# Optimization experiments

Hardware: AMD Instinct MI355X
Metric: run time of the kernel (lower is better)

The kernel has to match this reference:

```python
import jax, jax.numpy as jnp
import numpy as np

B, S, E, H = 2, 2048, 2048, 16
D = E // H  # head_out == qk_out (linformer_factor=1, attention_groups=0)
NEG = -1e30


def alibi_slopes(n_heads):
    # standard ALiBi slopes: 2^(-8*h/n_heads) for h = 1..n_heads
    return jnp.asarray(2.0 ** (-8.0 * np.arange(1, n_heads + 1) / n_heads), dtype=jnp.float32)


def setup_inputs() -> dict:
    key = jax.random.key(0)
    ks = jax.random.split(key, 5)
    sc = 0.02
    return {
        "x": jax.random.normal(ks[0], (B, S, E), dtype=jnp.float32),
        "Wq": jax.random.normal(ks[1], (E, E), dtype=jnp.float32) * sc,
        "Wk": jax.random.normal(ks[2], (E, E), dtype=jnp.float32) * sc,
        "Wv": jax.random.normal(ks[3], (E, E), dtype=jnp.float32) * sc,
        "Wo": jax.random.normal(ks[4], (E, E), dtype=jnp.float32) * sc,
        "bo": jnp.zeros((E,), dtype=jnp.float32),
    }


def reference(x, Wq, Wk, Wv, Wo, bo):
    b, s, e = x.shape
    # projections, split heads: [b, H, s, D]
    q = (x @ Wq).reshape(b, s, H, D).transpose(0, 2, 1, 3)
    k = (x @ Wk).reshape(b, s, H, D).transpose(0, 2, 1, 3)
    v = (x @ Wv).reshape(b, s, H, D).transpose(0, 2, 1, 3)
    scores = jnp.einsum("bhqd,bhkd->bhqk", q, k)
    # causal mask applied BEFORE scaling (as in original calc_attention)
    i = jnp.arange(s)[:, None]
    j = jnp.arange(s)[None, :]
    causal = j <= i  # [s, s]
    scores = jnp.where(causal[None, None], scores, NEG)
    # ALiBi bias: slope_h * (j - i), added before scaling
    bias = alibi_slopes(H)[:, None, None] * (j - i).astype(jnp.float32)  # [H, s, s]
    scores = scores + bias[None]
    scores = scores / jnp.sqrt(jnp.float32(D))
    w = jax.nn.softmax(scores, axis=-1)  # dropout rate 0.0 -> identity
    ctx = jnp.einsum("bhqk,bhkd->bqhd", w, v).reshape(b, s, e)
    return ctx @ Wo + bo
```

## Files before the change

### kernel.cpp

```cpp
#include <hip/hip_runtime.h>

#define BB 2
#define SS 2048
#define EE 2048
#define HH 16
#define DD 128
#define SE (3 * EE)

typedef __bf16 bf16x8 __attribute__((ext_vector_type(8)));
typedef unsigned short u16x8 __attribute__((ext_vector_type(8)));
typedef float f32x4 __attribute__((ext_vector_type(4)));

__device__ __forceinline__ unsigned short f32_to_bf16(float f) {
  unsigned int u = __builtin_bit_cast(unsigned int, f);
  u += 0x7FFFu + ((u >> 16) & 1u);
  return (unsigned short)(u >> 16);
}

__device__ __forceinline__ void gll16(const void* g, const void* lds) {
  __builtin_amdgcn_global_load_lds(
      (const __attribute__((address_space(1))) unsigned int*)g,
      (__attribute__((address_space(3))) unsigned int*)lds, 16, 0, 0);
}

__device__ __forceinline__ bf16x8 lds_frag(const unsigned short* p) {
  return __builtin_bit_cast(bf16x8, *(const u16x8*)p);
}

__global__ void k_cast_bf16(const float* __restrict__ x, unsigned short* __restrict__ y) {
  int i = blockIdx.x * 256 + threadIdx.x;
  float4 v = ((const float4*)x)[i];
  ushort4 o;
  o.x = f32_to_bf16(v.x); o.y = f32_to_bf16(v.y);
  o.z = f32_to_bf16(v.z); o.w = f32_to_bf16(v.w);
  ((ushort4*)y)[i] = o;
}

__global__ void k_transpose_w4(const float* __restrict__ W0, const float* __restrict__ W1,
                               const float* __restrict__ W2, const float* __restrict__ W3,
                               unsigned short* __restrict__ WtBase) {
  const float* W = blockIdx.z == 0 ? W0 : blockIdx.z == 1 ? W1 : blockIdx.z == 2 ? W2 : W3;
  unsigned short* Wt = WtBase + (size_t)blockIdx.z * EE * EE;
  __shared__ float tile[32][33];
  int n0 = blockIdx.x * 32, k0 = blockIdx.y * 32;
  int t = threadIdx.x, r = t >> 5, c = t & 31;
  for (int i = 0; i < 32; i += 8)
    tile[r + i][c] = W[(size_t)(k0 + r + i) * EE + n0 + c];
  __syncthreads();
  for (int i = 0; i < 32; i += 8)
    Wt[(size_t)(n0 + r + i) * EE + k0 + c] = f32_to_bf16(tile[c][r + i]);
}

__global__ void k_transpose_v(const unsigned short* __restrict__ QKV, unsigned short* __restrict__ Vt) {
  __shared__ unsigned short tile[32][33];
  int s0 = blockIdx.x * 32, d0 = blockIdx.y * 32, bh = blockIdx.z;
  int b = bh >> 4, h = bh & 15;
  int t = threadIdx.x, r = t >> 5, c = t & 31;
  for (int i = 0; i < 32; i += 8)
    tile[r + i][c] = QKV[(size_t)(b * SS + s0 + r + i) * SE + 2 * EE + h * DD + d0 + c];
  __syncthreads();
  for (int i = 0; i < 32; i += 8)
    Vt[(size_t)(bh * DD + d0 + r + i) * SS + s0 + c] = tile[c][r + i];
}

template <int OUTF32>
__global__ __launch_bounds__(256, 4) void k_gemm_bt(
    const unsigned short* __restrict__ A, const unsigned short* __restrict__ Bt,
    void* __restrict__ Cout, const float* __restrict__ bias, int K, int N) {
  __shared__ unsigned short As[128 * 64];
  __shared__ unsigned short Bs[128 * 64];
  const int tid = threadIdx.x;
  const int l = tid & 63, w = tid >> 6;
  const int m0 = blockIdx.y * 128, n0 = blockIdx.x * 128;
  const int tm = l & 15, qc = l >> 4;
  const int swz = tm & 7;
  const int m_base = (w >> 1) * 64, n_base = (w & 1) * 64;
  f32x4 acc[4][4] = {};

  for (int k0 = 0; k0 < K; k0 += 64) {
    for (int is = 0; is < 4; ++is) {
      int o = (w * 4 + is) * 1024 + l * 16;
      int row = o >> 7, slot = (o >> 4) & 7;
      int c = slot ^ (row & 7);
      gll16(&A[(size_t)(m0 + row) * K + k0 + c * 8], ((const char*)As) + o);
      gll16(&Bt[(size_t)(n0 + row) * K + k0 + c * 8], ((const char*)Bs) + o);
    }
    __syncthreads();
    for (int ks = 0; ks < 2; ++ks) {
      bf16x8 a[4], b[4];
      for (int im = 0; im < 4; ++im)
        a[im] = lds_frag(&As[(m_base + im * 16 + tm) * 64 + (((ks * 4 + qc) ^ swz) << 3)]);
      for (int in = 0; in < 4; ++in)
        b[in] = lds_frag(&Bs[(n_base + in * 16 + tm) * 64 + (((ks * 4 + qc) ^ swz) << 3)]);
      for (int im = 0; im < 4; ++im)
        for (int in = 0; in < 4; ++in)
          acc[im][in] = __builtin_amdgcn_mfma_f32_16x16x32_bf16(a[im], b[in], acc[im][in], 0, 0, 0);
    }
    __syncthreads();
  }

  for (int im = 0; im < 4; ++im)
    for (int in = 0; in < 4; ++in)
      for (int r = 0; r < 4; ++r) {
        int row = m0 + m_base + im * 16 + (l >> 4) * 4 + r;
        int col = n0 + n_base + in * 16 + tm;
        if (OUTF32)
          ((float*)Cout)[(size_t)row * N + col] = acc[im][in][r] + bias[col];
        else
          ((unsigned short*)Cout)[(size_t)row * N + col] = f32_to_bf16(acc[im][in][r]);
      }
}

__global__ __launch_bounds__(256, 2) void k_attn(
    const unsigned short* __restrict__ QKV, const unsigned short* __restrict__ Vt,
    unsigned short* __restrict__ ctx) {
  __shared__ unsigned short smem[40960];
  const int tid = threadIdx.x;
  const int l = tid & 63, w = tid >> 6;
  const int tm = l & 15, qc = l >> 4;
  const int bh = blockIdx.x, b = bh >> 4, h = bh & 15;
  const int rank = blockIdx.y;
  const int t = (rank < 8) ? (15 - rank) : (rank - 8);
  const int q0 = t * 128;
  const int n_it = 2 * t + 2;
  const float c1 = 0.12751676f;
  const float slopeL = exp2f(-0.5f * (float)(h + 1)) * c1;

  const unsigned short* Qg = QKV + h * DD;
  const unsigned short* Kg = QKV + EE + h * DD;
  const unsigned short* Vg = Vt + (size_t)bh * DD * SS;
  unsigned short* Ps = smem + 32768 + w * 2048;

  for (int is = 0; is < 8; ++is) {
    int idx = (w * 8 + is) * 64 + l;
    int row = idx >> 4, c = (idx & 15) ^ (row & 7);
    gll16(&Qg[(size_t)(b * SS + q0 + row) * SE + c * 8], ((char*)smem) + 32768 + idx * 16);
  }
  for (int is = 0; is < 4; ++is) {
    int idx = (w * 4 + is) * 64 + l;
    int kr = idx >> 4, kc = (idx & 15) ^ (kr & 7);
    gll16(&Kg[(size_t)(b * SS + kr) * SE + kc * 8], ((char*)smem) + idx * 16);
    int vr = idx >> 3, vc = (idx & 7) ^ (vr & 7);
    gll16(&Vg[(size_t)vr * SS + vc * 8], ((char*)smem) + 16384 + idx * 16);
  }
  __syncthreads();
  bf16x8 qf[2][4];
  for (int im = 0; im < 2; ++im)
    for (int kk = 0; kk < 4; ++kk) {
      int row = w * 32 + im * 16 + tm;
      qf[im][kk] = lds_frag(&smem[16384 + (row * 16 + ((kk * 4 + qc) ^ (tm & 7))) * 8]);
    }
  __syncthreads();

  float lr[2][4] = {};
  f32x4 o[2][8] = {};

  for (int it = 0; it < n_it; ++it) {
    const int kt = it * 64;
    const unsigned short* K_ = smem + (it & 1) * 16384;
    const unsigned short* V_ = K_ + 8192;
    if (it + 1 < n_it) {
      char* Kd = ((char*)smem) + ((it + 1) & 1) * 32768;
      int ktn = kt + 64;
      for (int is = 0; is < 4; ++is) {
        int idx = (w * 4 + is) * 64 + l;
        int kr = idx >> 4, kc = (idx & 15) ^ (kr & 7);
        gll16(&Kg[(size_t)(b * SS + ktn + kr) * SE + kc * 8], Kd + idx * 16);
        int vr = idx >> 3, vc = (idx & 7) ^ (vr & 7);
        gll16(&Vg[(size_t)vr * SS + ktn + vc * 8], Kd + 16384 + idx * 16);
      }
    }
    const bool full = (kt + 64 <= q0);

    for (int kn = 0; kn < 4; ++kn) {
      bf16x8 kf[4];
      for (int kk = 0; kk < 4; ++kk) {
        int row = kn * 16 + tm;
        kf[kk] = lds_frag(&K_[(row * 16 + ((kk * 4 + qc) ^ (tm & 7))) * 8]);
      }
      f32x4 a0 = {}, a1 = {};
      for (int kk = 0; kk < 4; ++kk) {
        a0 = __builtin_amdgcn_mfma_f32_16x16x32_bf16(qf[0][kk], kf[kk], a0, 0, 0, 0);
        a1 = __builtin_amdgcn_mfma_f32_16x16x32_bf16(qf[1][kk], kf[kk], a1, 0, 0, 0);
      }
      const int j = kt + kn * 16 + tm;
      for (int im = 0; im < 2; ++im) {
        const f32x4 av = im ? a1 : a0;
        const int ibase = q0 + w * 32 + im * 16 + qc * 4;
        for (int r = 0; r < 4; ++r) {
          int d = j - (ibase + r);
          float arg = av[r] * c1 + slopeL * (float)d;
          if (!full && d > 0) arg = -1e30f;
          float p = __builtin_amdgcn_exp2f(arg);
          lr[im][r] += p;
          unsigned int u = __builtin_bit_cast(unsigned int, p);
          int prow = im * 16 + qc * 4 + r;
          int pslot = (kn * 2 + (tm >> 3)) ^ (prow & 7);
          Ps[(prow * 8 + pslot) * 8 + (tm & 7)] = (unsigned short)(u >> 16);
        }
      }
    }
    asm volatile("s_waitcnt lgkmcnt(0)" ::: "memory");
    bf16x8 pf[2][2];
    for (int im = 0; im < 2; ++im)
      for (int k2 = 0; k2 < 2; ++k2) {
        int prow = im * 16 + tm;
        pf[im][k2] = lds_frag(&Ps[(prow * 8 + ((k2 * 4 + qc) ^ (tm & 7))) * 8]);
      }
    for (int dc = 0; dc < 8; ++dc) {
      int vrow = dc * 16 + tm;
      bf16x8 vf0 = lds_frag(&V_[(vrow * 8 + (qc ^ (tm & 7))) * 8]);
      bf16x8 vf1 = lds_frag(&V_[(vrow * 8 + ((4 + qc) ^ (tm & 7))) * 8]);
      o[0][dc] = __builtin_amdgcn_mfma_f32_16x16x32_bf16(pf[0][0], vf0, o[0][dc], 0, 0, 0);
      o[0][dc] = __builtin_amdgcn_mfma_f32_16x16x32_bf16(pf[0][1], vf1, o[0][dc], 0, 0, 0);
      o[1][dc] = __builtin_amdgcn_mfma_f32_16x16x32_bf16(pf[1][0], vf0, o[1][dc], 0, 0, 0);
      o[1][dc] = __builtin_amdgcn_mfma_f32_16x16x32_bf16(pf[1][1], vf1, o[1][dc], 0, 0, 0);
    }
    __syncthreads();
  }

  for (int im = 0; im < 2; ++im)
    for (int r = 0; r < 4; ++r) {
      float s = lr[im][r];
      for (int off = 8; off >= 1; off >>= 1) s += __shfl_xor(s, off, 64);
      float inv = 1.0f / s;
      int i = q0 + w * 32 + im * 16 + qc * 4 + r;
      for (int dc = 0; dc < 8; ++dc)
        ctx[(size_t)(b * SS + i) * EE + h * DD + dc * 16 + tm] =
            f32_to_bf16(o[im][dc][r] * inv);
    }
}

extern "C" void kernel_launch(void* const* d_in, const int* in_sizes, int n_in,
                              void* d_out, int out_size, void* d_ws, size_t ws_size,
                              hipStream_t stream) {
  const float* x  = (const float*)d_in[0];
  const float* Wq = (const float*)d_in[1];
  const float* Wk = (const float*)d_in[2];
  const float* Wv = (const float*)d_in[3];
  const float* Wo = (const float*)d_in[4];
  const float* bo = (const float*)d_in[5];
  float* out = (float*)d_out;

  const size_t XE = (size_t)BB * SS * EE;
  const size_t WE = (size_t)EE * EE;
  unsigned short* ws   = (unsigned short*)d_ws;
  unsigned short* xb   = ws;
  unsigned short* WqT  = xb + XE;
  unsigned short* WoT  = WqT + 3 * WE;
  unsigned short* QKVb = WoT + WE;
  unsigned short* Vt   = QKVb + 3 * XE;
  unsigned short* ctx  = xb;

  k_cast_bf16<<<XE / 1024, 256, 0, stream>>>(x, xb);
  k_transpose_w4<<<dim3(EE / 32, EE / 32, 4), 256, 0, stream>>>(Wq, Wk, Wv, Wo, WqT);

  dim3 gqkv(SE / 128, (BB * SS) / 128);
  k_gemm_bt<0><<<gqkv, 256, 0, stream>>>(xb, WqT, QKVb, nullptr, EE, SE);

  k_transpose_v<<<dim3(SS / 32, DD / 32, BB * HH), 256, 0, stream>>>(QKVb, Vt);
  k_attn<<<dim3(BB * HH, SS / 128), 256, 0, stream>>>(QKVb, Vt, ctx);

  dim3 gg(EE / 128, (BB * SS) / 128);
  k_gemm_bt<1><<<gg, 256, 0, stream>>>(ctx, WoT, out, bo, EE, EE);
}
```

Measured before the change: 368.5 us.

## Rewrite projection GEMMs with 256x128 tiles and triple-buffered LDS prefetch

```diff
diff --git a/kernel.cpp b/kernel.cpp
--- a/kernel.cpp
+++ b/kernel.cpp
@@ -63,47 +63,111 @@
     Vt[(size_t)(bh * DD + d0 + r + i) * SS + s0 + c] = tile[c][r + i];
 }
 
+#define GBM 256
+#define GBN 128
+#define GBK 64
+#define NBUF 3
+
 template <int OUTF32>
-__global__ __launch_bounds__(256, 4) void k_gemm_bt(
+__global__ __launch_bounds__(512, 2) void k_gemm_bt8(
     const unsigned short* __restrict__ A, const unsigned short* __restrict__ Bt,
     void* __restrict__ Cout, const float* __restrict__ bias, int K, int N) {
-  __shared__ unsigned short As[128 * 64];
-  __shared__ unsigned short Bs[128 * 64];
+  __shared__ unsigned short As[NBUF * GBM * GBK];
+  __shared__ unsigned short Bs[NBUF * GBN * GBK];
   const int tid = threadIdx.x;
   const int l = tid & 63, w = tid >> 6;
-  const int m0 = blockIdx.y * 128, n0 = blockIdx.x * 128;
+  const int wr = w >> 1, wc = w & 1;
+  const int m0 = blockIdx.y * GBM, n0 = blockIdx.x * GBN;
   const int tm = l & 15, qc = l >> 4;
   const int swz = tm & 7;
-  const int m_base = (w >> 1) * 64, n_base = (w & 1) * 64;
   f32x4 acc[4][4] = {};
 
-  for (int k0 = 0; k0 < K; k0 += 64) {
-    for (int is = 0; is < 4; ++is) {
-      int o = (w * 4 + is) * 1024 + l * 16;
-      int row = o >> 7, slot = (o >> 4) & 7;
-      int c = slot ^ (row & 7);
-      gll16(&A[(size_t)(m0 + row) * K + k0 + c * 8], ((const char*)As) + o);
-      gll16(&Bt[(size_t)(n0 + row) * K + k0 + c * 8], ((const char*)Bs) + o);
-    }
-    __syncthreads();
-    for (int ks = 0; ks < 2; ++ks) {
-      bf16x8 a[4], b[4];
-      for (int im = 0; im < 4; ++im)
-        a[im] = lds_frag(&As[(m_base + im * 16 + tm) * 64 + (((ks * 4 + qc) ^ swz) << 3)]);
+  const unsigned short* srcA[4];
+  const unsigned short* srcB[2];
+  int ldsA[4], ldsB[2];
+  for (int u = 0; u < 4; ++u) {
+    int idx = u * 512 + tid;
+    int row = idx >> 3, c = (idx & 7) ^ (row & 7);
+    srcA[u] = A + (size_t)(m0 + row) * K + c * 8;
+    ldsA[u] = idx * 16;
+  }
+  for (int u = 0; u < 2; ++u) {
+    int idx = u * 512 + tid;
+    int row = idx >> 3, c = (idx & 7) ^ (row & 7);
+    srcB[u] = Bt + (size_t)(n0 + row) * K + c * 8;
+    ldsB[u] = idx * 16;
+  }
+
+  const int NT = K >> 6;
+
+  for (int tt = 0; tt < 2; ++tt) {
+    char* Ad = (char*)As + tt * (GBM * GBK * 2);
+    char* Bd = (char*)Bs + tt * (GBN * GBK * 2);
+    const int k0 = tt * GBK;
+    for (int u = 0; u < 4; ++u) gll16(srcA[u] + k0, Ad + ldsA[u]);
+    for (int u = 0; u < 2; ++u) gll16(srcB[u] + k0, Bd + ldsB[u]);
+  }
+  asm volatile("s_waitcnt vmcnt(6)" ::: "memory");
+  __builtin_amdgcn_s_barrier();
+
+  int cur = 0;
+  for (int t = 0; t < NT; ++t) {
+    const unsigned short* Ab = As + cur * (GBM * GBK);
+    const unsigned short* Bb = Bs + cur * (GBN * GBK);
+    int nxt = cur - 1; if (nxt < 0) nxt = NBUF - 1;
+    char* And = (char*)As + nxt * (GBM * GBK * 2);
+    char* Bnd = (char*)Bs + nxt * (GBN * GBK * 2);
+    const bool pf = (t + 2 < NT);
+    const int kpf = (t + 2) * GBK;
+
+    bf16x8 a0[4], b0[4];
+    for (int im = 0; im < 4; ++im)
+      a0[im] = lds_frag(&Ab[(wr * 64 + im * 16 + tm) * 64 + ((qc ^ swz) << 3)]);
+    for (int in = 0; in < 4; ++in)
+      b0[in] = lds_frag(&Bb[(wc * 64 + in * 16 + tm) * 64 + ((qc ^ swz) << 3)]);
+    if (pf) {
+      gll16(srcA[0] + kpf, And + ldsA[0]);
+      gll16(srcA[1] + kpf, And + ldsA[1]);
+      gll16(srcB[0] + kpf, Bnd + ldsB[0]);
+    }
+    __builtin_amdgcn_s_barrier();
+    __builtin_amdgcn_s_setprio(1);
+    for (int im = 0; im < 4; ++im)
       for (int in = 0; in < 4; ++in)
-        b[in] = lds_frag(&Bs[(n_base + in * 16 + tm) * 64 + (((ks * 4 + qc) ^ swz) << 3)]);
-      for (int im = 0; im < 4; ++im)
-        for (int in = 0; in < 4; ++in)
-          acc[im][in] = __builtin_amdgcn_mfma_f32_16x16x32_bf16(a[im], b[in], acc[im][in], 0, 0, 0);
-    }
-    __syncthreads();
+        acc[im][in] = __builtin_amdgcn_mfma_f32_16x16x32_bf16(a0[im], b0[in], acc[im][in], 0, 0, 0);
+    __builtin_amdgcn_s_setprio(0);
+    __builtin_amdgcn_s_barrier();
+
+    bf16x8 a1[4], b1[4];
+    for (int im = 0; im < 4; ++im)
+      a1[im] = lds_frag(&Ab[(wr * 64 + im * 16 + tm) * 64 + (((4 + qc) ^ swz) << 3)]);
+    for (int in = 0; in < 4; ++in)
+      b1[in] = lds_frag(&Bb[(wc * 64 + in * 16 + tm) * 64 + (((4 + qc) ^ swz) << 3)]);
+    if (pf) {
+      gll16(srcA[2] + kpf, And + ldsA[2]);
+      gll16(srcA[3] + kpf, And + ldsA[3]);
+      gll16(srcB[1] + kpf, Bnd + ldsB[1]);
+    }
+    __builtin_amdgcn_s_barrier();
+    __builtin_amdgcn_s_setprio(1);
+    for (int im = 0; im < 4; ++im)
+      for (int in = 0; in < 4; ++in)
+        acc[im][in] = __builtin_amdgcn_mfma_f32_16x16x32_bf16(a1[im], b1[in], acc[im][in], 0, 0, 0);
+    __builtin_amdgcn_s_setprio(0);
+    if (t + 1 < NT) {
+      if (pf) asm volatile("s_waitcnt vmcnt(6)" ::: "memory");
+      else    asm volatile("s_waitcnt vmcnt(0)" ::: "memory");
+      __builtin_amdgcn_s_barrier();
+    }
+    cur = nxt == 0 ? (NBUF - 1) : (nxt - 1);
+    cur = (t + 1) % NBUF;
   }
 
   for (int im = 0; im < 4; ++im)
     for (int in = 0; in < 4; ++in)
       for (int r = 0; r < 4; ++r) {
-        int row = m0 + m_base + im * 16 + (l >> 4) * 4 + r;
-        int col = n0 + n_base + in * 16 + tm;
+        int row = m0 + wr * 64 + im * 16 + qc * 4 + r;
+        int col = n0 + wc * 64 + in * 16 + tm;
         if (OUTF32)
           ((float*)Cout)[(size_t)row * N + col] = acc[im][in][r] + bias[col];
         else
@@ -255,12 +319,12 @@
   k_cast_bf16<<<XE / 1024, 256, 0, stream>>>(x, xb);
   k_transpose_w4<<<dim3(EE / 32, EE / 32, 4), 256, 0, stream>>>(Wq, Wk, Wv, Wo, WqT);
 
-  dim3 gqkv(SE / 128, (BB * SS) / 128);
-  k_gemm_bt<0><<<gqkv, 256, 0, stream>>>(xb, WqT, QKVb, nullptr, EE, SE);
+  dim3 gqkv(SE / GBN, (BB * SS) / GBM);
+  k_gemm_bt8<0><<<gqkv, 512, 0, stream>>>(xb, WqT, QKVb, nullptr, EE, SE);
 
   k_transpose_v<<<dim3(SS / 32, DD / 32, BB * HH), 256, 0, stream>>>(QKVb, Vt);
   k_attn<<<dim3(BB * HH, SS / 128), 256, 0, stream>>>(QKVb, Vt, ctx);
 
-  dim3 gg(EE / 128, (BB * SS) / 128);
-  k_gemm_bt<1><<<gg, 256, 0, stream>>>(ctx, WoT, out, bo, EE, EE);
-}
+  dim3 gg(EE / GBN, (BB * SS) / GBM);
+  k_gemm_bt8<1><<<gg, 512, 0, stream>>>(ctx, WoT, out, bo, EE, EE);
+}
```

After: 372.1 us. Within noise of the previous version (+1.0%).

## Triple-buffer GEMM K-tiles with async LDS loads and vmcnt waits

Applied to the files above, without the earlier changes.

```diff
diff --git a/kernel.cpp b/kernel.cpp
--- a/kernel.cpp
+++ b/kernel.cpp
@@ -64,39 +64,65 @@
 }
 
 template <int OUTF32>
-__global__ __launch_bounds__(256, 4) void k_gemm_bt(
+__global__ __launch_bounds__(256, 3) void k_gemm_bt(
     const unsigned short* __restrict__ A, const unsigned short* __restrict__ Bt,
     void* __restrict__ Cout, const float* __restrict__ bias, int K, int N) {
-  __shared__ unsigned short As[128 * 64];
-  __shared__ unsigned short Bs[128 * 64];
+  __shared__ unsigned short As[3 * 128 * 32];
+  __shared__ unsigned short Bs[3 * 128 * 32];
   const int tid = threadIdx.x;
   const int l = tid & 63, w = tid >> 6;
   const int m0 = blockIdx.y * 128, n0 = blockIdx.x * 128;
   const int tm = l & 15, qc = l >> 4;
-  const int swz = tm & 7;
   const int m_base = (w >> 1) * 64, n_base = (w & 1) * 64;
   f32x4 acc[4][4] = {};
 
-  for (int k0 = 0; k0 < K; k0 += 64) {
-    for (int is = 0; is < 4; ++is) {
-      int o = (w * 4 + is) * 1024 + l * 16;
-      int row = o >> 7, slot = (o >> 4) & 7;
-      int c = slot ^ (row & 7);
-      gll16(&A[(size_t)(m0 + row) * K + k0 + c * 8], ((const char*)As) + o);
-      gll16(&Bt[(size_t)(n0 + row) * K + k0 + c * 8], ((const char*)Bs) + o);
-    }
-    __syncthreads();
-    for (int ks = 0; ks < 2; ++ks) {
-      bf16x8 a[4], b[4];
-      for (int im = 0; im < 4; ++im)
-        a[im] = lds_frag(&As[(m_base + im * 16 + tm) * 64 + (((ks * 4 + qc) ^ swz) << 3)]);
+  const unsigned short* srcA[2];
+  const unsigned short* srcB[2];
+  int ldsOff[2];
+  for (int u = 0; u < 2; ++u) {
+    int idx = u * 256 + tid;
+    int row = idx >> 2, ch = idx & 3;
+    srcA[u] = A + (size_t)(m0 + row) * K + ch * 8;
+    srcB[u] = Bt + (size_t)(n0 + row) * K + ch * 8;
+    ldsOff[u] = idx * 16;
+  }
+  const int NH = K >> 5;
+
+  for (int hh = 0; hh < 2; ++hh)
+    for (int u = 0; u < 2; ++u) {
+      gll16(srcA[u] + hh * 32, ((char*)As) + hh * 8192 + ldsOff[u]);
+      gll16(srcB[u] + hh * 32, ((char*)Bs) + hh * 8192 + ldsOff[u]);
+    }
+  asm volatile("s_waitcnt vmcnt(4)" ::: "memory");
+  __builtin_amdgcn_s_barrier();
+
+  int cur = 0;
+  for (int h = 0; h < NH; ++h) {
+    int nx2 = cur + 2; if (nx2 >= 3) nx2 -= 3;
+    const bool pf = (h + 2 < NH);
+    if (pf) {
+      const int ko = (h + 2) * 32;
+      for (int u = 0; u < 2; ++u) {
+        gll16(srcA[u] + ko, ((char*)As) + nx2 * 8192 + ldsOff[u]);
+        gll16(srcB[u] + ko, ((char*)Bs) + nx2 * 8192 + ldsOff[u]);
+      }
+    }
+    const unsigned short* Ab = As + cur * 4096;
+    const unsigned short* Bb = Bs + cur * 4096;
+    bf16x8 a[4], b[4];
+    for (int im = 0; im < 4; ++im)
+      a[im] = lds_frag(&Ab[(m_base + im * 16 + tm) * 32 + qc * 8]);
+    for (int in = 0; in < 4; ++in)
+      b[in] = lds_frag(&Bb[(n_base + in * 16 + tm) * 32 + qc * 8]);
+    for (int im = 0; im < 4; ++im)
       for (int in = 0; in < 4; ++in)
-        b[in] = lds_frag(&Bs[(n_base + in * 16 + tm) * 64 + (((ks * 4 + qc) ^ swz) << 3)]);
-      for (int im = 0; im < 4; ++im)
-        for (int in = 0; in < 4; ++in)
-          acc[im][in] = __builtin_amdgcn_mfma_f32_16x16x32_bf16(a[im], b[in], acc[im][in], 0, 0, 0);
-    }
-    __syncthreads();
+        acc[im][in] = __builtin_amdgcn_mfma_f32_16x16x32_bf16(a[im], b[in], acc[im][in], 0, 0, 0);
+    if (h + 1 < NH) {
+      if (pf) asm volatile("s_waitcnt vmcnt(4)" ::: "memory");
+      else    asm volatile("s_waitcnt vmcnt(0)" ::: "memory");
+      __builtin_amdgcn_s_barrier();
+    }
+    cur = cur + 1; if (cur >= 3) cur -= 3;
   }
 
   for (int im = 0; im < 4; ++im)
```

Result: slower. 390.8 us (+6.0%).

## Double-buffer GEMM LDS tiles, hoist V fragment loads, add MFMA priority hints

Applied to the files above, without the earlier changes.

```diff
diff --git a/kernel.cpp b/kernel.cpp
--- a/kernel.cpp
+++ b/kernel.cpp
@@ -64,11 +64,11 @@
 }
 
 template <int OUTF32>
-__global__ __launch_bounds__(256, 4) void k_gemm_bt(
+__global__ __launch_bounds__(256, 2) void k_gemm_bt(
     const unsigned short* __restrict__ A, const unsigned short* __restrict__ Bt,
     void* __restrict__ Cout, const float* __restrict__ bias, int K, int N) {
-  __shared__ unsigned short As[128 * 64];
-  __shared__ unsigned short Bs[128 * 64];
+  __shared__ unsigned short As[2 * 128 * 64];
+  __shared__ unsigned short Bs[2 * 128 * 64];
   const int tid = threadIdx.x;
   const int l = tid & 63, w = tid >> 6;
   const int m0 = blockIdx.y * 128, n0 = blockIdx.x * 128;
@@ -77,24 +77,48 @@
   const int m_base = (w >> 1) * 64, n_base = (w & 1) * 64;
   f32x4 acc[4][4] = {};
 
-  for (int k0 = 0; k0 < K; k0 += 64) {
-    for (int is = 0; is < 4; ++is) {
-      int o = (w * 4 + is) * 1024 + l * 16;
-      int row = o >> 7, slot = (o >> 4) & 7;
-      int c = slot ^ (row & 7);
-      gll16(&A[(size_t)(m0 + row) * K + k0 + c * 8], ((const char*)As) + o);
-      gll16(&Bt[(size_t)(n0 + row) * K + k0 + c * 8], ((const char*)Bs) + o);
-    }
-    __syncthreads();
+  const unsigned short* srcA[4];
+  const unsigned short* srcB[4];
+  int ldsOff[4];
+  for (int is = 0; is < 4; ++is) {
+    int idx = (w * 4 + is) * 64 + l;
+    int row = idx >> 3, c = (idx & 7) ^ (row & 7);
+    srcA[is] = A + (size_t)(m0 + row) * K + c * 8;
+    srcB[is] = Bt + (size_t)(n0 + row) * K + c * 8;
+    ldsOff[is] = idx * 16;
+  }
+  const int NT = K >> 6;
+
+  for (int is = 0; is < 4; ++is) {
+    gll16(srcA[is], (char*)As + ldsOff[is]);
+    gll16(srcB[is], (char*)Bs + ldsOff[is]);
+  }
+  __syncthreads();
+
+  for (int t = 0; t < NT; ++t) {
+    const int cur = t & 1;
+    if (t + 1 < NT) {
+      const int ko = (t + 1) * 64;
+      char* Ad = (char*)As + (cur ^ 1) * 16384;
+      char* Bd = (char*)Bs + (cur ^ 1) * 16384;
+      for (int is = 0; is < 4; ++is) {
+        gll16(srcA[is] + ko, Ad + ldsOff[is]);
+        gll16(srcB[is] + ko, Bd + ldsOff[is]);
+      }
+    }
+    const unsigned short* Ab = As + cur * 8192;
+    const unsigned short* Bb = Bs + cur * 8192;
     for (int ks = 0; ks < 2; ++ks) {
       bf16x8 a[4], b[4];
       for (int im = 0; im < 4; ++im)
-        a[im] = lds_frag(&As[(m_base + im * 16 + tm) * 64 + (((ks * 4 + qc) ^ swz) << 3)]);
+        a[im] = lds_frag(&Ab[(m_base + im * 16 + tm) * 64 + (((ks * 4 + qc) ^ swz) << 3)]);
       for (int in = 0; in < 4; ++in)
-        b[in] = lds_frag(&Bs[(n_base + in * 16 + tm) * 64 + (((ks * 4 + qc) ^ swz) << 3)]);
+        b[in] = lds_frag(&Bb[(n_base + in * 16 + tm) * 64 + (((ks * 4 + qc) ^ swz) << 3)]);
+      __builtin_amdgcn_s_setprio(1);
       for (int im = 0; im < 4; ++im)
         for (int in = 0; in < 4; ++in)
           acc[im][in] = __builtin_amdgcn_mfma_f32_16x16x32_bf16(a[im], b[in], acc[im][in], 0, 0, 0);
+      __builtin_amdgcn_s_setprio(0);
     }
     __syncthreads();
   }
@@ -125,6 +149,7 @@
   const int n_it = 2 * t + 2;
   const float c1 = 0.12751676f;
   const float slopeL = exp2f(-0.5f * (float)(h + 1)) * c1;
+  const float sr1 = slopeL, sr2 = slopeL * 2.0f, sr3 = slopeL * 3.0f;
 
   const unsigned short* Qg = QKV + h * DD;
   const unsigned short* Kg = QKV + EE + h * DD;
@@ -172,25 +197,43 @@
     }
     const bool full = (kt + 64 <= q0);
 
+    bf16x8 vf0[8], vf1[8];
+#pragma unroll
     for (int kn = 0; kn < 4; ++kn) {
       bf16x8 kf[4];
+#pragma unroll
       for (int kk = 0; kk < 4; ++kk) {
         int row = kn * 16 + tm;
         kf[kk] = lds_frag(&K_[(row * 16 + ((kk * 4 + qc) ^ (tm & 7))) * 8]);
       }
+      {
+        const int dcA = kn * 2, dcB = kn * 2 + 1;
+        const int vrA = dcA * 16 + tm, vrB = dcB * 16 + tm;
+        vf0[dcA] = lds_frag(&V_[(vrA * 8 + (qc ^ (tm & 7))) * 8]);
+        vf1[dcA] = lds_frag(&V_[(vrA * 8 + ((4 + qc) ^ (tm & 7))) * 8]);
+        vf0[dcB] = lds_frag(&V_[(vrB * 8 + (qc ^ (tm & 7))) * 8]);
+        vf1[dcB] = lds_frag(&V_[(vrB * 8 + ((4 + qc) ^ (tm & 7))) * 8]);
+      }
       f32x4 a0 = {}, a1 = {};
+      __builtin_amdgcn_s_setprio(1);
+#pragma unroll
       for (int kk = 0; kk < 4; ++kk) {
         a0 = __builtin_amdgcn_mfma_f32_16x16x32_bf16(qf[0][kk], kf[kk], a0, 0, 0, 0);
         a1 = __builtin_amdgcn_mfma_f32_16x16x32_bf16(qf[1][kk], kf[kk], a1, 0, 0, 0);
       }
+      __builtin_amdgcn_s_setprio(0);
       const int j = kt + kn * 16 + tm;
+#pragma unroll
       for (int im = 0; im < 2; ++im) {
         const f32x4 av = im ? a1 : a0;
         const int ibase = q0 + w * 32 + im * 16 + qc * 4;
+        const int dj = j - ibase;
+        const float bse = slopeL * (float)dj;
+#pragma unroll
         for (int r = 0; r < 4; ++r) {
-          int d = j - (ibase + r);
-          float arg = av[r] * c1 + slopeL * (float)d;
-          if (!full && d > 0) arg = -1e30f;
+          const float srr = (r == 0) ? 0.0f : (r == 1) ? sr1 : (r == 2) ? sr2 : sr3;
+          float arg = av[r] * c1 + (bse - srr);
+          if (!full && dj > r) arg = -1e30f;
           float p = __builtin_amdgcn_exp2f(arg);
           lr[im][r] += p;
           unsigned int u = __builtin_bit_cast(unsigned int, p);
@@ -202,20 +245,22 @@
     }
     asm volatile("s_waitcnt lgkmcnt(0)" ::: "memory");
     bf16x8 pf[2][2];
+#pragma unroll
     for (int im = 0; im < 2; ++im)
+#pragma unroll
       for (int k2 = 0; k2 < 2; ++k2) {
         int prow = im * 16 + tm;
         pf[im][k2] = lds_frag(&Ps[(prow * 8 + ((k2 * 4 + qc) ^ (tm & 7))) * 8]);
       }
+    __builtin_amdgcn_s_setprio(1);
+#pragma unroll
     for (int dc = 0; dc < 8; ++dc) {
-      int vrow = dc * 16 + tm;
-      bf16x8 vf0 = lds_frag(&V_[(vrow * 8 + (qc ^ (tm & 7))) * 8]);
-      bf16x8 vf1 = lds_frag(&V_[(vrow * 8 + ((4 + qc) ^ (tm & 7))) * 8]);
-      o[0][dc] = __builtin_amdgcn_mfma_f32_16x16x32_bf16(pf[0][0], vf0, o[0][dc], 0, 0, 0);
-      o[0][dc] = __builtin_amdgcn_mfma_f32_16x16x32_bf16(pf[0][1], vf1, o[0][dc], 0, 0, 0);
-      o[1][dc] = __builtin_amdgcn_mfma_f32_16x16x32_bf16(pf[1][0], vf0, o[1][dc], 0, 0, 0);
-      o[1][dc] = __builtin_amdgcn_mfma_f32_16x16x32_bf16(pf[1][1], vf1, o[1][dc], 0, 0, 0);
-    }
+      o[0][dc] = __builtin_amdgcn_mfma_f32_16x16x32_bf16(pf[0][0], vf0[dc], o[0][dc], 0, 0, 0);
+      o[0][dc] = __builtin_amdgcn_mfma_f32_16x16x32_bf16(pf[0][1], vf1[dc], o[0][dc], 0, 0, 0);
+      o[1][dc] = __builtin_amdgcn_mfma_f32_16x16x32_bf16(pf[1][0], vf0[dc], o[1][dc], 0, 0, 0);
+      o[1][dc] = __builtin_amdgcn_mfma_f32_16x16x32_bf16(pf[1][1], vf1[dc], o[1][dc], 0, 0, 0);
+    }
+    __builtin_amdgcn_s_setprio(0);
     __syncthreads();
   }
 
```

New measurement: 459.5 us. 24.7% more time.
